# Kernel tuning notes

Measured on AMD Instinct MI355X. Metric: run time of the kernel, lower is better.

## Reference

```python
import jax, jax.numpy as jnp
import numpy as np

L = 3      # gat_layer_num
H = 4      # multi_num (attention heads)
N = 26     # nodes (keypoints)
F = 26     # features per node
B = 16384  # batch


def setup_inputs() -> dict:
    key = jax.random.key(0)
    ks = jax.random.split(key, 8)
    s = 1.0 / np.sqrt(F)
    x = jax.random.normal(ks[0], (B, N, F), dtype=jnp.float32)
    W = jax.random.normal(ks[1], (L, H, F, F), dtype=jnp.float32) * s
    a_src = jax.random.normal(ks[2], (L, H, F), dtype=jnp.float32) * s
    a_dst = jax.random.normal(ks[3], (L, H, F), dtype=jnp.float32) * s
    W1 = jax.random.normal(ks[4], (N * F, 256), dtype=jnp.float32) * (1.0 / np.sqrt(N * F))
    b1 = jnp.zeros((256,), dtype=jnp.float32)
    W2 = jax.random.normal(ks[5], (256, 3), dtype=jnp.float32) * (1.0 / np.sqrt(256))
    b2 = jnp.zeros((3,), dtype=jnp.float32)
    return {"dummy": 0, "x": x, "W": W, "a_src": a_src, "a_dst": a_dst,
            "W1": W1, "b1": b1, "W2": W2, "b2": b2}


def _gat_layer(x, W_l, a_src_l, a_dst_l):
    # x: [B,N,F]; W_l: [H,F,F]; a_*: [H,F]
    h = jnp.einsum('bnf,hfo->bhno', x, W_l)          # [B,H,N,F]
    s_src = jnp.einsum('bhnf,hf->bhn', h, a_src_l)    # [B,H,N]
    s_dst = jnp.einsum('bhnf,hf->bhn', h, a_dst_l)    # [B,H,N]
    e = s_src[..., :, None] + s_dst[..., None, :]     # [B,H,N,N]
    e = jax.nn.leaky_relu(e, negative_slope=0.2)
    alpha = jax.nn.softmax(e, axis=-1)                # softmax over neighbors j
    out = jnp.einsum('bhij,bhjf->bhif', alpha, h)     # [B,H,N,F]
    out = out.mean(axis=1)                            # average heads -> [B,N,F]
    return jax.nn.elu(out)


def reference(dummy, x, W, a_src, a_dst, W1, b1, W2, b2):
    for l in range(L):
        x = _gat_layer(x, W[l], a_src[l], a_dst[l])
    flat = x.reshape(x.shape[0], -1)                  # [B, N*F]
    hdn = jax.nn.leaky_relu(flat @ W1 + b1, negative_slope=0.2)
    return hdn @ W2 + b2                              # [B, 3]
```

## Files before the change

kernel.cpp:

```cpp
#include <hip/hip_runtime.h>

typedef __attribute__((ext_vector_type(8))) short s16x8;
typedef __attribute__((ext_vector_type(4))) float f32x4;
typedef unsigned short u16;
typedef unsigned int   u32;

#define MFMA16(a,b,c) __builtin_amdgcn_mfma_f32_16x16x32_bf16((a),(b),(c),0,0,0)

__device__ __forceinline__ float bf2f(u16 u){
  u32 x = ((u32)u) << 16; float f; __builtin_memcpy(&f, &x, 4); return f;
}
__device__ __forceinline__ float bflo(u32 v){
  u32 x = v << 16; float f; __builtin_memcpy(&f, &x, 4); return f;
}
__device__ __forceinline__ float bfhi(u32 v){
  u32 x = v & 0xFFFF0000u; float f; __builtin_memcpy(&f, &x, 4); return f;
}
__device__ __forceinline__ u16 f2bf(float f){
  u32 x; __builtin_memcpy(&x, &f, 4);
  x += 0x7FFFu + ((x >> 16) & 1u);
  return (u16)(x >> 16);
}
#if defined(__has_builtin) && __has_builtin(__builtin_amdgcn_cvt_pk_bf16_f32)
__device__ __forceinline__ u32 pack2(float a, float b){
  return __builtin_bit_cast(u32, __builtin_amdgcn_cvt_pk_bf16_f32(a, b));
}
#else
__device__ __forceinline__ u32 pack2(float a, float b){
  return (u32)f2bf(a) | ((u32)f2bf(b) << 16);
}
#endif
#if defined(__has_builtin) && __has_builtin(__builtin_amdgcn_exp2f)
__device__ __forceinline__ float fexp2(float x){ return __builtin_amdgcn_exp2f(x); }
#else
extern "C" __device__ float __ocml_native_exp2_f32(float);
__device__ __forceinline__ float fexp2(float x){ return __ocml_native_exp2_f32(x); }
#endif


__global__ __launch_bounds__(256) void prep_kernel(
    const float* __restrict__ W, const float* __restrict__ a_src,
    const float* __restrict__ a_dst, const float* __restrict__ W1,
    u16* __restrict__ w1t, u16* __restrict__ wp)
{
  const int t = threadIdx.x;
  if (blockIdx.x < 352){
    const int k = blockIdx.x * 2;
    const int n = t;
    float v0 = 0.f, v1 = 0.f;
    if (k < 676)     v0 = W1[(size_t)k*256 + n];
    if (k + 1 < 676) v1 = W1[(size_t)(k+1)*256 + n];
    const int ntile = n >> 4, lm = n & 15;
    const int kc = k >> 5, q16 = (k >> 3) & 3, j = k & 7;
    u16* dst = w1t + ((((size_t)ntile*22 + kc)*64 + q16*16 + lm) << 3) + j;
    *(u32*)dst = pack2(v0, v1);
  } else {
    const int lh = blockIdx.x - 352;
    const float* Wlh = W + lh*676;
    u16* dst = wp + lh*32*40;
    for (int e = t; e < 1280; e += 256) dst[e] = 0;
    __syncthreads();
    for (int e = t; e < 676; e += 256){
      int f = e/26, o = e%26;
      dst[o*40 + f] = f2bf(0.25f * Wlh[f*26 + o]);
    }
    if (t < 52){
      int sel = t/26, f = t%26;
      const float* av = (sel ? a_dst : a_src) + lh*26;
      float acc = 0.f;
      #pragma unroll
      for (int o = 0; o < 26; ++o) acc += Wlh[f*26 + o]*av[o];
      dst[(26 + sel)*40 + f] = f2bf(1.4426950408889634f * acc);
    }
  }
}

__global__ __launch_bounds__(256, 4) void gat_kernel(
    const float* __restrict__ x, const u16* __restrict__ wp,
    u16* __restrict__ xf)
{
  __shared__ __align__(16) u16 xs [128*36];
  __shared__ __align__(16) u16 hsT[4*28*136];

  const int tid  = threadIdx.x;
  const int w    = tid >> 6;
  const int lane = tid & 63;
  const int q    = lane >> 4;
  const int lm   = lane & 15;
  const int lmc  = (lm < 11) ? lm : 11;
  const int b0   = blockIdx.x * 4;
  const float L2E = 1.4426950408889634f;

  const bool pm01 = (lm == 11) && (q == 3);
  const bool pm23 = (lm == 11) && (q >= 2);

  for (int e = tid; e < 2304; e += 256) ((u32*)xs)[e] = 0;
  __syncthreads();
  for (int pp = tid; pp < 1352; pp += 256){
    int b = pp/338, r2 = pp%338, n = r2/13, p = r2%13;
    float2 v = *(const float2*)&x[(b0 + b)*676 + n*26 + 2*p];
    *(u32*)&xs[(b*32 + n)*36 + 2*p] = pack2(v.x, v.y);
  }

  for (int l = 0; l < 3; ++l){
    __syncthreads();

    {
      s16x8 bfr0 = *(const s16x8*)&wp[((l*4 + w)*32      + lm)*40 + q*8];
      s16x8 bfr1 = *(const s16x8*)&wp[((l*4 + w)*32 + 16 + lm)*40 + q*8];
      #pragma unroll
      for (int t = 0; t < 8; ++t){
        s16x8 af = *(const s16x8*)&xs[(t*16 + lm)*36 + q*8];
        f32x4 z = {0.f,0.f,0.f,0.f};
        f32x4 d0 = MFMA16(af, bfr0, z);
        f32x4 d1 = MFMA16(af, bfr1, z);
        const int gr0 = t*16 + q*4;
        if (t & 1){
          d1[0] = pm01 ? -1e30f : d1[0];
          d1[1] = pm01 ? -1e30f : d1[1];
          d1[2] = pm23 ? -1e30f : d1[2];
          d1[3] = pm23 ? -1e30f : d1[3];
        }
        { uint2 uu; uu.x = pack2(d0[0], d0[1]); uu.y = pack2(d0[2], d0[3]);
          *(uint2*)&hsT[(w*28 + lm)*136 + gr0] = uu; }
        if (lm < 12){
          uint2 uu; uu.x = pack2(d1[0], d1[1]); uu.y = pack2(d1[2], d1[3]);
          *(uint2*)&hsT[(w*28 + 16 + lm)*136 + gr0] = uu; }
      }
    }
    __syncthreads();

    {
      f32x4 acc00 = {0,0,0,0}, acc01 = acc00, acc10 = acc00, acc11 = acc00;
      const int j0  = q*8;
      const int b32 = w*32;
      #pragma unroll
      for (int h = 0; h < 4; ++h){
        s16x8 am0 = *(const s16x8*)&hsT[(h*28      + lm )*136 + b32 + j0];
        s16x8 am1 = *(const s16x8*)&hsT[(h*28 + 16 + lmc)*136 + b32 + j0];
        uint4 sdv = *(const uint4*)&hsT[(h*28 + 27      )*136 + b32 + j0];
        float sd2[8];
        sd2[0] = bflo(sdv.x); sd2[1] = bfhi(sdv.x);
        sd2[2] = bflo(sdv.y); sd2[3] = bfhi(sdv.y);
        sd2[4] = bflo(sdv.z); sd2[5] = bfhi(sdv.z);
        sd2[6] = bflo(sdv.w); sd2[7] = bfhi(sdv.w);
        #pragma unroll
        for (int nt = 0; nt < 2; ++nt){
          int i = nt*16 + lm;
          float si2 = bf2f(hsT[(h*28 + 26)*136 + b32 + i]);
          float p[8]; float loc = 0.f;
          #pragma unroll
          for (int jj = 0; jj < 8; ++jj){
            float e = si2 + sd2[jj];
            e = fmaxf(e, 0.2f*e);
            float pv = fexp2(e);
            p[jj] = pv; loc += pv;
          }
          float tot = loc;
          tot += __shfl_xor(tot, 16);
          tot += __shfl_xor(tot, 32);
          float rinv = __builtin_amdgcn_rcpf(tot);
          uint4 bu = { pack2(p[0]*rinv, p[1]*rinv), pack2(p[2]*rinv, p[3]*rinv),
                       pack2(p[4]*rinv, p[5]*rinv), pack2(p[6]*rinv, p[7]*rinv) };
          s16x8 bfrag = __builtin_bit_cast(s16x8, bu);
          if (nt == 0){ acc00 = MFMA16(am0, bfrag, acc00);
                        acc10 = MFMA16(am1, bfrag, acc10); }
          else        { acc01 = MFMA16(am0, bfrag, acc01);
                        acc11 = MFMA16(am1, bfrag, acc11); }
        }
      }
      #pragma unroll
      for (int nt = 0; nt < 2; ++nt){
        int i = nt*16 + lm;
        if (i < 26){
          int rowb = (w*32 + i)*36;
          #pragma unroll
          for (int mt = 0; mt < 2; ++mt){
            f32x4 a = (mt == 0) ? (nt == 0 ? acc00 : acc01)
                                : (nt == 0 ? acc10 : acc11);
            int f0 = mt*16 + q*4;
            float v0 = a[0], v1 = a[1], v2 = a[2], v3 = a[3];
            v0 = (v0 > 0.f) ? v0 : (fexp2(v0*L2E) - 1.f);
            v1 = (v1 > 0.f) ? v1 : (fexp2(v1*L2E) - 1.f);
            v2 = (v2 > 0.f) ? v2 : (fexp2(v2*L2E) - 1.f);
            v3 = (v3 > 0.f) ? v3 : (fexp2(v3*L2E) - 1.f);
            if (f0 <= 20){
              uint2 uu; uu.x = pack2(v0, v1); uu.y = pack2(v2, v3);
              *(uint2*)&xs[rowb + f0] = uu;
            } else if (f0 == 24){
              *(u32*)&xs[rowb + 24] = pack2(v0, v1);
            }
          }
        }
      }
    }
  }
  __syncthreads();
  {
    const int mtile = b0 >> 4;
    const int lrow0 = b0 & 15;
    u16* dstb = xf + (size_t)mtile*22*64*8;
    for (int e = tid; e < 1408; e += 256){
      int chunk = e >> 4;
      int u     = e & 15;
      int kc = chunk >> 2, q16 = chunk & 3;
      int bb = u >> 2;
      int j2 = (u & 3) * 2;
      int k  = kc*32 + q16*8 + j2;
      u32 v = 0;
      if (k < 676){ int n = k/26, f = k - n*26; v = *(const u32*)&xs[(bb*32 + n)*36 + f]; }
      *(u32*)&dstb[((kc*64 + q16*16 + lrow0 + bb) << 3) + j2] = v;
    }
  }
}

__global__ __launch_bounds__(256, 2) void mlp_kernel(
    const u16* __restrict__ xf, const u16* __restrict__ w1t,
    const float* __restrict__ b1, const float* __restrict__ w2,
    const float* __restrict__ b2, float* __restrict__ out)
{
  __shared__ float b1s[256];
  __shared__ float w2s[256*3];
  __shared__ float part[4*32*3];

  const int tid  = threadIdx.x;
  const int w    = tid >> 6;
  const int lane = tid & 63;
  const int q    = lane >> 4;
  const int lm   = lane & 15;
  const int m0   = blockIdx.x * 32;
  const int mt0  = blockIdx.x * 2;

  b1s[tid] = b1[tid];
  for (int e = tid; e < 768; e += 256) w2s[e] = w2[e];

  f32x4 acc[2][4];
  #pragma unroll
  for (int a = 0; a < 2; ++a)
    #pragma unroll
    for (int b = 0; b < 4; ++b) acc[a][b] = (f32x4){0.f,0.f,0.f,0.f};

  const u16* abase = xf  + ((size_t)mt0*22*64 + lane) * 8;
  const u16* bbase = w1t + (((size_t)w*4)*22*64 + lane) * 8;

  s16x8 af[2], bf[4], afn[2], bfn[4];
  #pragma unroll
  for (int mt = 0; mt < 2; ++mt) af[mt] = *(const s16x8*)(abase + (size_t)(mt*22)*64*8);
  #pragma unroll
  for (int nt = 0; nt < 4; ++nt) bf[nt] = *(const s16x8*)(bbase + (size_t)(nt*22)*64*8);

  #pragma unroll
  for (int kc = 0; kc < 22; ++kc){
    if (kc < 21){
      #pragma unroll
      for (int mt = 0; mt < 2; ++mt)
        afn[mt] = *(const s16x8*)(abase + (size_t)(mt*22 + kc + 1)*64*8);
      #pragma unroll
      for (int nt = 0; nt < 4; ++nt)
        bfn[nt] = *(const s16x8*)(bbase + (size_t)(nt*22 + kc + 1)*64*8);
    }
    #pragma unroll
    for (int mt = 0; mt < 2; ++mt)
      #pragma unroll
      for (int nt = 0; nt < 4; ++nt)
        acc[mt][nt] = MFMA16(af[mt], bf[nt], acc[mt][nt]);
    #pragma unroll
    for (int mt = 0; mt < 2; ++mt) af[mt] = afn[mt];
    #pragma unroll
    for (int nt = 0; nt < 4; ++nt) bf[nt] = bfn[nt];
  }

  float b1l[4], w2l[4][3];
  #pragma unroll
  for (int nt = 0; nt < 4; ++nt){
    int col = w*64 + nt*16 + lm;
    b1l[nt] = b1s[col];
    w2l[nt][0] = w2s[col*3]; w2l[nt][1] = w2s[col*3+1]; w2l[nt][2] = w2s[col*3+2];
  }
  float po[2][4][3];
  #pragma unroll
  for (int mt = 0; mt < 2; ++mt)
    #pragma unroll
    for (int r = 0; r < 4; ++r){
      float s0 = 0.f, s1 = 0.f, s2 = 0.f;
      #pragma unroll
      for (int nt = 0; nt < 4; ++nt){
        float hv = acc[mt][nt][r] + b1l[nt];
        hv = (hv >= 0.f) ? hv : 0.2f*hv;
        s0 += hv*w2l[nt][0]; s1 += hv*w2l[nt][1]; s2 += hv*w2l[nt][2];
      }
      po[mt][r][0] = s0; po[mt][r][1] = s1; po[mt][r][2] = s2;
    }
  #pragma unroll
  for (int m = 1; m < 16; m <<= 1)
    #pragma unroll
    for (int mt = 0; mt < 2; ++mt)
      #pragma unroll
      for (int r = 0; r < 4; ++r)
        #pragma unroll
        for (int kk = 0; kk < 3; ++kk)
          po[mt][r][kk] += __shfl_xor(po[mt][r][kk], m);
  if (lm == 0){
    #pragma unroll
    for (int mt = 0; mt < 2; ++mt)
      #pragma unroll
      for (int r = 0; r < 4; ++r)
        #pragma unroll
        for (int kk = 0; kk < 3; ++kk)
          part[w*96 + (mt*16 + q*4 + r)*3 + kk] = po[mt][r][kk];
  }
  __syncthreads();
  if (tid < 96){
    int row = tid/3, kk = tid - row*3;
    float o = part[row*3 + kk] + part[96 + row*3 + kk]
            + part[192 + row*3 + kk] + part[288 + row*3 + kk] + b2[kk];
    out[(m0 + row)*3 + kk] = o;
  }
}

extern "C" void kernel_launch(void* const* d_in, const int* in_sizes, int n_in,
                              void* d_out, int out_size, void* d_ws, size_t ws_size,
                              hipStream_t stream)
{
  (void)in_sizes; (void)n_in; (void)out_size; (void)ws_size;
  const float* x     = (const float*)d_in[1];
  const float* W     = (const float*)d_in[2];
  const float* a_src = (const float*)d_in[3];
  const float* a_dst = (const float*)d_in[4];
  const float* W1    = (const float*)d_in[5];
  const float* b1    = (const float*)d_in[6];
  const float* W2    = (const float*)d_in[7];
  const float* b2    = (const float*)d_in[8];
  float* out = (float*)d_out;

  u16* xfinal = (u16*)d_ws;
  u16* w1t    = xfinal + (size_t)16384*704;
  u16* wp     = w1t    + 256*704;

  hipLaunchKernelGGL(prep_kernel, dim3(364),  dim3(256), 0, stream,
                     W, a_src, a_dst, W1, w1t, wp);
  hipLaunchKernelGGL(gat_kernel,  dim3(4096), dim3(256), 0, stream, x, wp, xfinal);
  hipLaunchKernelGGL(mlp_kernel,  dim3(512),  dim3(256), 0, stream,
                     xfinal, w1t, b1, W2, b2, out);
}
```

Baseline: 211.4 us.

## Make each wave own one sample across all heads to drop block barriers

Previously each wave computed one head's projection for all four samples in the block, which required block-wide barriers between the projection and attention phases. Now each wave computes all four heads for its own sample and writes only into its own slice of shared memory. This removes every __syncthreads in the layer loop and in the input staging. In exchange each wave loads four heads' weight fragments per layer instead of one, and it relies on the wave-private slices holding everything the attention phase reads.

```diff
diff --git a/kernel.cpp b/kernel.cpp
--- a/kernel.cpp
+++ b/kernel.cpp
@@ -89,51 +89,54 @@
   const int lm   = lane & 15;
   const int lmc  = (lm < 11) ? lm : 11;
   const int b0   = blockIdx.x * 4;
+  const int b32  = w*32;
   const float L2E = 1.4426950408889634f;
 
   const bool pm01 = (lm == 11) && (q == 3);
   const bool pm23 = (lm == 11) && (q >= 2);
 
-  for (int e = tid; e < 2304; e += 256) ((u32*)xs)[e] = 0;
-  __syncthreads();
-  for (int pp = tid; pp < 1352; pp += 256){
-    int b = pp/338, r2 = pp%338, n = r2/13, p = r2%13;
-    float2 v = *(const float2*)&x[(b0 + b)*676 + n*26 + 2*p];
-    *(u32*)&xs[(b*32 + n)*36 + 2*p] = pack2(v.x, v.y);
+  for (int e = lane; e < 576; e += 64) ((u32*)xs)[w*576 + e] = 0;
+  for (int pp = lane; pp < 338; pp += 64){
+    int n = pp/13, p = pp%13;
+    float2 v = *(const float2*)&x[(size_t)(b0 + w)*676 + n*26 + 2*p];
+    *(u32*)&xs[(b32 + n)*36 + 2*p] = pack2(v.x, v.y);
   }
 
   for (int l = 0; l < 3; ++l){
-    __syncthreads();
-
     {
-      s16x8 bfr0 = *(const s16x8*)&wp[((l*4 + w)*32      + lm)*40 + q*8];
-      s16x8 bfr1 = *(const s16x8*)&wp[((l*4 + w)*32 + 16 + lm)*40 + q*8];
-      #pragma unroll
-      for (int t = 0; t < 8; ++t){
-        s16x8 af = *(const s16x8*)&xs[(t*16 + lm)*36 + q*8];
+      s16x8 af0 = *(const s16x8*)&xs[(b32      + lm)*36 + q*8];
+      s16x8 af1 = *(const s16x8*)&xs[(b32 + 16 + lm)*36 + q*8];
+      #pragma unroll
+      for (int h = 0; h < 4; ++h){
+        s16x8 bfr0 = *(const s16x8*)&wp[((l*4 + h)*32      + lm)*40 + q*8];
+        s16x8 bfr1 = *(const s16x8*)&wp[((l*4 + h)*32 + 16 + lm)*40 + q*8];
         f32x4 z = {0.f,0.f,0.f,0.f};
-        f32x4 d0 = MFMA16(af, bfr0, z);
-        f32x4 d1 = MFMA16(af, bfr1, z);
-        const int gr0 = t*16 + q*4;
-        if (t & 1){
-          d1[0] = pm01 ? -1e30f : d1[0];
-          d1[1] = pm01 ? -1e30f : d1[1];
-          d1[2] = pm23 ? -1e30f : d1[2];
-          d1[3] = pm23 ? -1e30f : d1[3];
+        f32x4 d00 = MFMA16(af0, bfr0, z);
+        f32x4 d10 = MFMA16(af1, bfr0, z);
+        f32x4 d01 = MFMA16(af0, bfr1, z);
+        f32x4 d11 = MFMA16(af1, bfr1, z);
+        d11[0] = pm01 ? -1e30f : d11[0];
+        d11[1] = pm01 ? -1e30f : d11[1];
+        d11[2] = pm23 ? -1e30f : d11[2];
+        d11[3] = pm23 ? -1e30f : d11[3];
+        const int rlo = (h*28 + lm)*136 + b32 + q*4;
+        { uint2 uu; uu.x = pack2(d00[0], d00[1]); uu.y = pack2(d00[2], d00[3]);
+          *(uint2*)&hsT[rlo] = uu; }
+        { uint2 uu; uu.x = pack2(d10[0], d10[1]); uu.y = pack2(d10[2], d10[3]);
+          *(uint2*)&hsT[rlo + 16] = uu; }
+        if (lm < 12){
+          const int rhi = (h*28 + 16 + lm)*136 + b32 + q*4;
+          { uint2 uu; uu.x = pack2(d01[0], d01[1]); uu.y = pack2(d01[2], d01[3]);
+            *(uint2*)&hsT[rhi] = uu; }
+          { uint2 uu; uu.x = pack2(d11[0], d11[1]); uu.y = pack2(d11[2], d11[3]);
+            *(uint2*)&hsT[rhi + 16] = uu; }
         }
-        { uint2 uu; uu.x = pack2(d0[0], d0[1]); uu.y = pack2(d0[2], d0[3]);
-          *(uint2*)&hsT[(w*28 + lm)*136 + gr0] = uu; }
-        if (lm < 12){
-          uint2 uu; uu.x = pack2(d1[0], d1[1]); uu.y = pack2(d1[2], d1[3]);
-          *(uint2*)&hsT[(w*28 + 16 + lm)*136 + gr0] = uu; }
       }
     }
-    __syncthreads();
 
     {
       f32x4 acc00 = {0,0,0,0}, acc01 = acc00, acc10 = acc00, acc11 = acc00;
-      const int j0  = q*8;
-      const int b32 = w*32;
+      const int j0 = q*8;
       #pragma unroll
       for (int h = 0; h < 4; ++h){
         s16x8 am0 = *(const s16x8*)&hsT[(h*28      + lm )*136 + b32 + j0];
@@ -173,7 +176,7 @@
       for (int nt = 0; nt < 2; ++nt){
         int i = nt*16 + lm;
         if (i < 26){
-          int rowb = (w*32 + i)*36;
+          int rowb = (b32 + i)*36;
           #pragma unroll
           for (int mt = 0; mt < 2; ++mt){
             f32x4 a = (mt == 0) ? (nt == 0 ? acc00 : acc01)
```

Measured after the change: 209.5 us. Within noise of the previous version (-0.9%).
